# Kernel tuning notes

Hardware: AMD Instinct MI355X
Metric: run time of the kernel (lower is better)

The kernel has to match this reference:

```python
import jax, jax.numpy as jnp
import numpy as np
from functools import partial

B, C, D, H, W = 2, 96, 64, 64, 64
HALF = C // 2
EPS = 1e-5


def _dwconv3d(x, w, b):
    # x: [B, half, D, H, W]; w: [half, 1, 3, 3, 3] depthwise; b: [half]
    y = jax.lax.conv_general_dilated(
        x, w, window_strides=(1, 1, 1), padding=((1, 1), (1, 1), (1, 1)),
        dimension_numbers=('NCDHW', 'OIDHW', 'NCDHW'),
        feature_group_count=x.shape[1])
    return y + b[None, :, None, None, None]


def _conv1x1(x, w, b):
    # pointwise conv == channel GEMM; w: [Cout, Cin], b: [Cout]
    return jnp.einsum('oc,bcdhw->bodhw', w, x) + b[None, :, None, None, None]


def setup_inputs() -> dict:
    key = jax.random.key(0)
    ks = jax.random.split(key, 12)
    s = 0.02
    return {
        'x': jax.random.normal(ks[0], (B, C, D, H, W), dtype=jnp.float32),
        'norm_gamma': jnp.ones((C,), jnp.float32),
        'norm_beta': jnp.zeros((C,), jnp.float32),
        'in_w': jax.random.normal(ks[1], (C, C), jnp.float32) * s,
        'in_b': jnp.zeros((C,), jnp.float32),
        'conv_ssm_w': jax.random.normal(ks[2], (HALF, 1, 3, 3, 3), jnp.float32) * s,
        'conv_ssm_b': jnp.zeros((HALF,), jnp.float32),
        'mamba_w': jax.random.normal(ks[3], (HALF, 1, 3, 3, 3), jnp.float32) * s,
        'mamba_b': jnp.zeros((HALF,), jnp.float32),
        'conv_sym_w': jax.random.normal(ks[4], (HALF, 1, 3, 3, 3), jnp.float32) * s,
        'conv_sym_b': jnp.zeros((HALF,), jnp.float32),
        'out_w': jax.random.normal(ks[5], (C, C), jnp.float32) * s,
        'out_b': jnp.zeros((C,), jnp.float32),
    }


def reference(x, norm_gamma, norm_beta, in_w, in_b,
              conv_ssm_w, conv_ssm_b, mamba_w, mamba_b,
              conv_sym_w, conv_sym_b, out_w, out_b):
    residual = x
    # InstanceNorm3d (affine): normalize over spatial dims per (batch, channel)
    mean = jnp.mean(x, axis=(2, 3, 4), keepdims=True)
    var = jnp.var(x, axis=(2, 3, 4), keepdims=True)
    xn = (x - mean) * jax.lax.rsqrt(var + EPS)
    xn = xn * norm_gamma[None, :, None, None, None] + norm_beta[None, :, None, None, None]
    # shared 1x1 projection then split into two branches
    xp = _conv1x1(xn, in_w, in_b)
    x1, x2 = xp[:, :HALF], xp[:, HALF:]
    # SSM path: depthwise conv -> SiLU -> (fallback) depthwise conv 'mamba'
    x1 = jax.nn.silu(_dwconv3d(x1, conv_ssm_w, conv_ssm_b))
    x1 = _dwconv3d(x1, mamba_w, mamba_b)
    # symmetric conv path
    x2 = jax.nn.silu(_dwconv3d(x2, conv_sym_w, conv_sym_b))
    out = _conv1x1(jnp.concatenate([x1, x2], axis=1), out_w, out_b)
    return out + residual
```

## Files before the change

### kernel.cpp

```cpp
#include <hip/hip_runtime.h>
#include <hip/hip_bf16.h>

using u16 = unsigned short;
using u32 = unsigned int;
typedef __attribute__((ext_vector_type(8))) short bf16x8;
typedef __attribute__((ext_vector_type(4))) float f32x4;

#define DEVFN __device__ __forceinline__

static constexpr int Sn = 64*64*64;
static constexpr float EPS_ = 1e-5f;

DEVFN float lo2f(u32 u){ union { u32 i; float f; } v; v.i = u << 16; return v.f; }
DEVFN float hi2f(u32 u){ union { u32 i; float f; } v; v.i = u & 0xffff0000u; return v.f; }
DEVFN float b2f(u16 u){ union { u32 i; float f; } v; v.i = ((u32)u) << 16; return v.f; }
DEVFN u16 f2b(float f){
  union { float f; u32 i; } v; v.f = f;
  u32 r = v.i + 0x7fffu + ((v.i >> 16) & 1u);
  return (u16)(r >> 16);
}
DEVFN void unpack8(uint4 v, float* f){
  f[0]=lo2f(v.x); f[1]=hi2f(v.x);
  f[2]=lo2f(v.y); f[3]=hi2f(v.y);
  f[4]=lo2f(v.z); f[5]=hi2f(v.z);
  f[6]=lo2f(v.w); f[7]=hi2f(v.w);
}
DEVFN void unpack4(uint2 v, float* f){
  f[0]=lo2f(v.x); f[1]=hi2f(v.x);
  f[2]=lo2f(v.y); f[3]=hi2f(v.y);
}
DEVFN void load8f(const float* p, float* f){
  float4 a = *reinterpret_cast<const float4*>(p);
  float4 b = *reinterpret_cast<const float4*>(p + 4);
  f[0]=a.x; f[1]=a.y; f[2]=a.z; f[3]=a.w;
  f[4]=b.x; f[5]=b.y; f[6]=b.z; f[7]=b.w;
}

__global__ __launch_bounds__(256) void k_stats_partial(
    const float* __restrict__ x, float2* __restrict__ psum, u16* __restrict__ xb){
  int bid = blockIdx.x;
  int bc = bid >> 2, chunk = bid & 3;
  size_t base = (size_t)bc * Sn + (size_t)chunk * (Sn/4);
  const float* p = x + base;
  u16* q = xb + base;
  float s = 0.f, s2 = 0.f;
  int t = threadIdx.x;
  #pragma unroll 4
  for (int k = 0; k < 32; ++k){
    size_t off = (size_t)k*2048 + t*8;
    float f[8]; load8f(p + off, f);
    u16 ob[8];
    #pragma unroll
    for (int j=0;j<8;j++){ s += f[j]; s2 += f[j]*f[j]; ob[j] = f2b(f[j]); }
    *reinterpret_cast<uint4*>(q + off) = *reinterpret_cast<const uint4*>(ob);
  }
  #pragma unroll
  for (int off=32; off; off>>=1){ s += __shfl_down(s, off); s2 += __shfl_down(s2, off); }
  __shared__ float rs[4], rs2[4];
  int wid = t >> 6;
  if ((t & 63) == 0){ rs[wid]=s; rs2[wid]=s2; }
  __syncthreads();
  if (t == 0){
    psum[bid] = make_float2(rs[0]+rs[1]+rs[2]+rs[3], rs2[0]+rs2[1]+rs2[2]+rs2[3]);
  }
}

__global__ __launch_bounds__(192) void k_fold(
    const float2* __restrict__ psum,
    const float* __restrict__ gamma, const float* __restrict__ beta,
    const float* __restrict__ in_w, const float* __restrict__ in_b,
    const float* __restrict__ out_w,
    u16* __restrict__ W2pad ,
    u16* __restrict__ W3pad ,
    float* __restrict__ bias2 ){
  __shared__ float scl[192], shf[192];
  int t = threadIdx.x;
  {
    float s=0.f, s2=0.f;
    #pragma unroll
    for (int k=0;k<4;k++){ float2 v = psum[t*4+k]; s += v.x; s2 += v.y; }
    float inv = 1.f / (float)Sn;
    float mean = s * inv;
    float var  = s2 * inv - mean*mean;
    int c = t % 96;
    float sc = gamma[c] * rsqrtf(var + EPS_);
    scl[t] = sc;
    shf[t] = beta[c] - mean * sc;
  }
  __syncthreads();
  int b = t / 96, o = t % 96;
  float acc = in_b[o];
  for (int c=0;c<96;c++){
    float w = in_w[o*96 + c];
    int bc = b*96 + c;
    W2pad[(size_t)(b*96 + o)*104 + c] = f2b(w * scl[bc]);
    acc += w * shf[bc];
  }
  bias2[t] = acc;
  if (t < 96){
    for (int c=0;c<96;c++)
      W3pad[(size_t)t*104 + c] = f2b(out_w[t*96 + c]);
  }
}

template<int MODE>
__global__ __launch_bounds__(256, 4) void k_gemm(
    const u16*  __restrict__ xb,
    const u16*  __restrict__ y1,
    const u16*  __restrict__ y2,
    const u16*  __restrict__ Wpad,
    const float* __restrict__ bias,
    u16* __restrict__ dst16,
    float* __restrict__ dst32){
  __shared__ __attribute__((aligned(16))) u16 lds[18432];
  u16* Wl = lds;
  u16* X  = lds + 9984;
  const int t  = threadIdx.x;
  const int b  = blockIdx.x >> 12;
  const int s0 = (blockIdx.x & 4095) << 6;

  {
    const uint4* wsrc = reinterpret_cast<const uint4*>(Wpad + (MODE==0 ? (size_t)b*9984 : 0));
    uint4* wdst = reinterpret_cast<uint4*>(lds);
    #pragma unroll
    for (int i=0;i<5;i++){ int idx = i*256 + t; if (idx < 1248) wdst[idx] = wsrc[idx]; }
  }

  #pragma unroll
  for (int it=0; it<2; ++it){
    int task = it*256 + t;
    if (task < 384){
      int sp = task & 31, cblk = task >> 5;
      int s = sp*2;
      u16 rA[8], rB[8];
      #pragma unroll
      for (int j=0;j<8;j++){
        int c = cblk*8 + j;
        const u16* src;
        if (MODE==0)      src = xb + ((size_t)(b*96 + c))*Sn;
        else if (c < 48)  src = y1 + ((size_t)(b*48 + c))*Sn;
        else              src = y2 + ((size_t)(b*48 + (c-48)))*Sn;
        u32 v = *reinterpret_cast<const u32*>(src + s0 + s);
        rA[j] = (u16)v; rB[j] = (u16)(v >> 16);
      }
      *reinterpret_cast<uint4*>(&X[(size_t)s*132 + cblk*8]) = *reinterpret_cast<const uint4*>(rA);
      *reinterpret_cast<uint2*>(&X[(size_t)(s+1)*132 + cblk*8])     = *reinterpret_cast<const uint2*>(&rB[0]);
      *reinterpret_cast<uint2*>(&X[(size_t)(s+1)*132 + cblk*8 + 4]) = *reinterpret_cast<const uint2*>(&rB[4]);
    }
  }
  __syncthreads();

  const int w  = t >> 6;
  const int l  = t & 63;
  const int lc = l & 15, lr = l >> 4;

  f32x4 acc[6];
  #pragma unroll
  for (int m=0;m<6;m++)
    #pragma unroll
    for (int r=0;r<4;r++) acc[m][r] = 0.f;

  #pragma unroll
  for (int kk=0; kk<3; ++kk){
    const int kb = kk*4 + lr;
    bf16x8 xv;
    {
      const u16* px = &X[(size_t)(w*16 + lc)*132 + kb*8];
      uint2 p0 = *reinterpret_cast<const uint2*>(px);
      uint2 p1 = *reinterpret_cast<const uint2*>(px + 4);
      union { uint4 u; bf16x8 v; } cv;
      cv.u = make_uint4(p0.x, p0.y, p1.x, p1.y);
      xv = cv.v;
    }
    #pragma unroll
    for (int m=0;m<6;m++){
      bf16x8 a = *reinterpret_cast<const bf16x8*>(&Wl[(size_t)(16*m + lc)*104 + kb*8]);
      acc[m] = __builtin_amdgcn_mfma_f32_16x16x32_bf16(a, xv, acc[m], 0, 0, 0);
    }
  }
  __syncthreads();

  if (MODE==0){
    u16* eps = lds;
    #pragma unroll
    for (int m=0;m<6;m++){
      #pragma unroll
      for (int r=0;r<4;r++){
        int o = 16*m + lr*4 + r;
        eps[(size_t)o*72 + w*16 + lc] = f2b(acc[m][r] + bias[b*96 + o]);
      }
    }
    __syncthreads();
    #pragma unroll
    for (int i=0;i<3;i++){
      int idx = i*256 + t;
      int o = idx >> 3, qq = idx & 7;
      *reinterpret_cast<uint4*>(dst16 + ((size_t)(b*96 + o))*Sn + s0 + qq*8) =
          *reinterpret_cast<const uint4*>(&eps[(size_t)o*72 + qq*8]);
    }
  } else {
    float* eps = reinterpret_cast<float*>(lds);
    #pragma unroll
    for (int m=0;m<6;m++){
      #pragma unroll
      for (int r=0;r<4;r++){
        int o = 16*m + lr*4 + r;
        eps[(size_t)o*68 + w*16 + lc] = acc[m][r] + bias[o];
      }
    }
    __syncthreads();
    #pragma unroll
    for (int i=0;i<6;i++){
      int idx = i*256 + t;
      int o = idx >> 4, qq = idx & 15;
      size_t off = ((size_t)(b*96 + o))*Sn + s0 + qq*4;
      float4 v  = *reinterpret_cast<const float4*>(&eps[(size_t)o*68 + qq*4]);
      uint2 rv = *reinterpret_cast<const uint2*>(xb + off);
      float rf[4]; unpack4(rv, rf);
      v.x += rf[0]; v.y += rf[1]; v.z += rf[2]; v.w += rf[3];
      *reinterpret_cast<float4*>(dst32 + off) = v;
    }
  }
}

template<int SILU>
__global__ __launch_bounds__(256) void k_dw(
    const u16* __restrict__ src, int sCPB, int sCOff,
    u16* __restrict__ dst, int dCPB, int dCOff,
    const float* __restrict__ wts , const float* __restrict__ bias){
  int hw = blockIdx.x;
  int id = (hw & 7)*768 + (hw >> 3);
  int d = id & 63; int c = (id >> 6) % 48; int b = id / (48*64);
  int t = threadIdx.x;
  int h = t >> 2, w0 = (t & 3) * 16;
  float wf[27];
  const float* wp = wts + c*27;
  #pragma unroll
  for (int k=0;k<27;k++) wf[k] = wp[k];
  float acc[16];
  float bv = bias[c];
  #pragma unroll
  for (int j=0;j<16;j++) acc[j] = bv;
  const u16* sp = src + ((size_t)(b*sCPB + sCOff + c)) * Sn;
  #pragma unroll
  for (int dd=-1; dd<=1; dd++){
    int zd = d + dd; if (zd < 0 || zd > 63) continue;
    #pragma unroll
    for (int dh=-1; dh<=1; dh++){
      int zh = h + dh; if (zh < 0 || zh > 63) continue;
      const u16* row = sp + zd*4096 + zh*64 + w0;
      float m[16];
      unpack8(*reinterpret_cast<const uint4*>(row), m);
      unpack8(*reinterpret_cast<const uint4*>(row+8), m+8);
      float rl = __shfl_up(m[15], 1);
      float rr = __shfl_down(m[0], 1);
      if ((t & 3) == 0) rl = 0.f;
      if ((t & 3) == 3) rr = 0.f;
      const float* wk = &wf[(dd+1)*9 + (dh+1)*3];
      #pragma unroll
      for (int j=0;j<16;j++){
        float L = (j==0)  ? rl : m[j-1];
        float R = (j==15) ? rr : m[j+1];
        acc[j] += wk[0]*L + wk[1]*m[j] + wk[2]*R;
      }
    }
  }
  u16 ob[16];
  #pragma unroll
  for (int j=0;j<16;j++){
    float v = acc[j];
    if (SILU) v = v / (1.f + __expf(-v));
    ob[j] = f2b(v);
  }
  u16* dp = dst + ((size_t)(b*dCPB + dCOff + c)) * Sn + d*4096 + h*64 + w0;
  *reinterpret_cast<uint4*>(dp)   = *reinterpret_cast<const uint4*>(&ob[0]);
  *reinterpret_cast<uint4*>(dp+8) = *reinterpret_cast<const uint4*>(&ob[8]);
}

extern "C" void kernel_launch(void* const* d_in, const int* in_sizes, int n_in,
                              void* d_out, int out_size, void* d_ws, size_t ws_size,
                              hipStream_t stream){
  const float* x      = (const float*)d_in[0];
  const float* gamma  = (const float*)d_in[1];
  const float* beta   = (const float*)d_in[2];
  const float* in_w   = (const float*)d_in[3];
  const float* in_b   = (const float*)d_in[4];
  const float* ssm_w  = (const float*)d_in[5];
  const float* ssm_b  = (const float*)d_in[6];
  const float* mam_w  = (const float*)d_in[7];
  const float* mam_b  = (const float*)d_in[8];
  const float* sym_w  = (const float*)d_in[9];
  const float* sym_b  = (const float*)d_in[10];
  const float* out_w  = (const float*)d_in[11];
  const float* out_b  = (const float*)d_in[12];
  float* out = (float*)d_out;

  u16* du16 = (u16*)d_out;

  char* ws = (char*)d_ws;
  u16*    y2    = (u16*)ws;
  u16*    y1    = (u16*)(ws + 50331648);
  u16*    xb    = (u16*)(ws + 100663296);
  float2* psum  = (float2*)(ws + 201326592);
  u16*    W2pad = (u16*)(ws + 201326592 + 6144);
  u16*    W3pad = (u16*)(ws + 201326592 + 6144 + 39936);
  float*  bias2 = (float*)(ws + 201326592 + 6144 + 39936 + 19968);

  k_stats_partial<<<768, 256, 0, stream>>>(x, psum, xb);
  k_fold<<<1, 192, 0, stream>>>(psum, gamma, beta, in_w, in_b, out_w, W2pad, W3pad, bias2);
  k_gemm<0><<<8192, 256, 0, stream>>>(xb, nullptr, nullptr, W2pad, bias2, du16, nullptr);
  k_dw<1><<<6144, 256, 0, stream>>>(du16, 96, 48, y2, 48, 0, sym_w, sym_b);
  k_dw<1><<<6144, 256, 0, stream>>>(du16, 96, 0,  du16, 96, 192, ssm_w, ssm_b);
  k_dw<0><<<6144, 256, 0, stream>>>(du16, 96, 192, y1, 48, 0, mam_w, mam_b);
  k_gemm<1><<<8192, 256, 0, stream>>>(xb, y1, y2, W3pad, out_b, nullptr, out);
}
```

Baseline: 363.3 us.

## Stage depthwise conv halos in LDS, merge two dwconv launches, parallelize fold

The depthwise 3D conv kernel now loads three zero-padded depth planes into shared memory as fp32 and reads the 3x3 neighbourhood from LDS, where before each thread issued repeated global loads per tap and used shuffles for the edges. The first-stage ssm and sym depthwise convs are merged into one launch over 96 channels, with outputs routed to the right buffers. The single-block fold kernel is spread over 288 blocks, with a shared-memory reduction for the bias. The cost is a large LDS footprint per block, about 54KB, which limits occupancy, plus extra zero-fill and staging work.

```diff
diff --git a/kernel.cpp b/kernel.cpp
--- a/kernel.cpp
+++ b/kernel.cpp
@@ -65,7 +65,7 @@
   }
 }
 
-__global__ __launch_bounds__(192) void k_fold(
+__global__ __launch_bounds__(96) void k_fold(
     const float2* __restrict__ psum,
     const float* __restrict__ gamma, const float* __restrict__ beta,
     const float* __restrict__ in_w, const float* __restrict__ in_b,
@@ -73,33 +73,31 @@
     u16* __restrict__ W2pad ,
     u16* __restrict__ W3pad ,
     float* __restrict__ bias2 ){
-  __shared__ float scl[192], shf[192];
-  int t = threadIdx.x;
-  {
+  int blk = blockIdx.x;
+  int c = threadIdx.x;
+  if (blk < 192){
+    int b = blk / 96, o = blk - (blk/96)*96;
     float s=0.f, s2=0.f;
     #pragma unroll
-    for (int k=0;k<4;k++){ float2 v = psum[t*4+k]; s += v.x; s2 += v.y; }
+    for (int k=0;k<4;k++){ float2 v = psum[(b*96 + c)*4 + k]; s += v.x; s2 += v.y; }
     float inv = 1.f / (float)Sn;
     float mean = s * inv;
     float var  = s2 * inv - mean*mean;
-    int c = t % 96;
     float sc = gamma[c] * rsqrtf(var + EPS_);
-    scl[t] = sc;
-    shf[t] = beta[c] - mean * sc;
-  }
-  __syncthreads();
-  int b = t / 96, o = t % 96;
-  float acc = in_b[o];
-  for (int c=0;c<96;c++){
+    float sh = beta[c] - mean * sc;
     float w = in_w[o*96 + c];
-    int bc = b*96 + c;
-    W2pad[(size_t)(b*96 + o)*104 + c] = f2b(w * scl[bc]);
-    acc += w * shf[bc];
-  }
-  bias2[t] = acc;
-  if (t < 96){
-    for (int c=0;c<96;c++)
-      W3pad[(size_t)t*104 + c] = f2b(out_w[t*96 + c]);
+    W2pad[(size_t)(b*96 + o)*104 + c] = f2b(w * sc);
+    __shared__ float red[96];
+    red[c] = w * sh;
+    __syncthreads();
+    if (c == 0){
+      float a = in_b[o];
+      for (int i=0;i<96;i++) a += red[i];
+      bias2[b*96 + o] = a;
+    }
+  } else {
+    int o = blk - 192;
+    W3pad[(size_t)o*104 + c] = f2b(out_w[o*96 + c]);
   }
 }
 
@@ -223,15 +221,54 @@
   }
 }
 
-template<int SILU>
-__global__ __launch_bounds__(256) void k_dw(
+template<int SILU, int MERGED>
+__global__ __launch_bounds__(256) void k_dwl(
     const u16* __restrict__ src, int sCPB, int sCOff,
     u16* __restrict__ dst, int dCPB, int dCOff,
-    const float* __restrict__ wts , const float* __restrict__ bias){
+    u16* __restrict__ dst2,
+    const float* __restrict__ wtsA, const float* __restrict__ biasA,
+    const float* __restrict__ wtsB, const float* __restrict__ biasB){
   int hw = blockIdx.x;
-  int id = (hw & 7)*768 + (hw >> 3);
-  int d = id & 63; int c = (id >> 6) % 48; int b = id / (48*64);
-  int t = threadIdx.x;
+  int nchunk = MERGED ? 1536 : 768;
+  int id = (hw & 7)*nchunk + (hw >> 3);
+  int CC = MERGED ? 96 : 48;
+  int d = id & 63; int cc = (id >> 6) % CC; int b = id / (CC*64);
+  bool sym = MERGED && (cc >= 48);
+  int c = sym ? (cc - 48) : cc;
+  const float* wts  = sym ? wtsB  : wtsA;
+  const float* bias = sym ? biasB : biasA;
+  const int t = threadIdx.x;
+
+  __shared__ float S[4 + 3*66*68];
+
+  if (t < 4) S[t] = 0.f;
+  for (int z = t; z < 408; z += 256){
+    int s = z / 136, rm = z - s*136;
+    int r = (rm >= 68) ? 65 : 0; int wd = (rm >= 68) ? (rm - 68) : rm;
+    S[4 + s*4488 + r*68 + wd] = 0.f;
+  }
+  for (int z = t; z < 768; z += 256){
+    int s = z >> 8, i = z & 255; int h = i >> 2, wd = 64 + (i & 3);
+    S[4 + s*4488 + (h+1)*68 + wd] = 0.f;
+  }
+
+  const u16* plane = src + ((size_t)(b*sCPB + sCOff + cc)) * Sn;
+  #pragma unroll
+  for (int it = 0; it < 6; ++it){
+    int k = it*256 + t;
+    int s = k >> 9, i = k & 511;
+    int h = i >> 3, w8 = (i & 7) << 3;
+    int zd = d - 1 + s;
+    uint4 v = make_uint4(0u,0u,0u,0u);
+    if (zd >= 0 && zd <= 63)
+      v = *reinterpret_cast<const uint4*>(plane + zd*4096 + h*64 + w8);
+    float f[8]; unpack8(v, f);
+    float* q = &S[4 + s*4488 + (h+1)*68 + w8];
+    *reinterpret_cast<float4*>(q)   = *reinterpret_cast<const float4*>(&f[0]);
+    *reinterpret_cast<float4*>(q+4) = *reinterpret_cast<const float4*>(&f[4]);
+  }
+  __syncthreads();
+
   int h = t >> 2, w0 = (t & 3) * 16;
   float wf[27];
   const float* wp = wts + c*27;
@@ -241,22 +278,19 @@
   float bv = bias[c];
   #pragma unroll
   for (int j=0;j<16;j++) acc[j] = bv;
-  const u16* sp = src + ((size_t)(b*sCPB + sCOff + c)) * Sn;
-  #pragma unroll
-  for (int dd=-1; dd<=1; dd++){
-    int zd = d + dd; if (zd < 0 || zd > 63) continue;
-    #pragma unroll
-    for (int dh=-1; dh<=1; dh++){
-      int zh = h + dh; if (zh < 0 || zh > 63) continue;
-      const u16* row = sp + zd*4096 + zh*64 + w0;
+
+  #pragma unroll
+  for (int s=0;s<3;s++){
+    #pragma unroll
+    for (int dh=0;dh<3;dh++){
+      const float* row = &S[4 + s*4488 + (h+dh)*68 + w0];
       float m[16];
-      unpack8(*reinterpret_cast<const uint4*>(row), m);
-      unpack8(*reinterpret_cast<const uint4*>(row+8), m+8);
-      float rl = __shfl_up(m[15], 1);
-      float rr = __shfl_down(m[0], 1);
-      if ((t & 3) == 0) rl = 0.f;
-      if ((t & 3) == 3) rr = 0.f;
-      const float* wk = &wf[(dd+1)*9 + (dh+1)*3];
+      #pragma unroll
+      for (int q=0;q<4;q++)
+        *reinterpret_cast<float4*>(&m[q*4]) = *reinterpret_cast<const float4*>(row + q*4);
+      float rl = row[-1];
+      float rr = row[16];
+      const float* wk = &wf[s*9 + dh*3];
       #pragma unroll
       for (int j=0;j<16;j++){
         float L = (j==0)  ? rl : m[j-1];
@@ -265,6 +299,7 @@
       }
     }
   }
+
   u16 ob[16];
   #pragma unroll
   for (int j=0;j<16;j++){
@@ -272,7 +307,9 @@
     if (SILU) v = v / (1.f + __expf(-v));
     ob[j] = f2b(v);
   }
-  u16* dp = dst + ((size_t)(b*dCPB + dCOff + c)) * Sn + d*4096 + h*64 + w0;
+  u16* dp;
+  if (MERGED && sym) dp = dst2 + ((size_t)(b*48 + c)) * Sn + d*4096 + h*64 + w0;
+  else               dp = dst  + ((size_t)(b*dCPB + dCOff + c)) * Sn + d*4096 + h*64 + w0;
   *reinterpret_cast<uint4*>(dp)   = *reinterpret_cast<const uint4*>(&ob[0]);
   *reinterpret_cast<uint4*>(dp+8) = *reinterpret_cast<const uint4*>(&ob[8]);
 }
@@ -307,10 +344,9 @@
   float*  bias2 = (float*)(ws + 201326592 + 6144 + 39936 + 19968);
 
   k_stats_partial<<<768, 256, 0, stream>>>(x, psum, xb);
-  k_fold<<<1, 192, 0, stream>>>(psum, gamma, beta, in_w, in_b, out_w, W2pad, W3pad, bias2);
+  k_fold<<<288, 96, 0, stream>>>(psum, gamma, beta, in_w, in_b, out_w, W2pad, W3pad, bias2);
   k_gemm<0><<<8192, 256, 0, stream>>>(xb, nullptr, nullptr, W2pad, bias2, du16, nullptr);
-  k_dw<1><<<6144, 256, 0, stream>>>(du16, 96, 48, y2, 48, 0, sym_w, sym_b);
-  k_dw<1><<<6144, 256, 0, stream>>>(du16, 96, 0,  du16, 96, 192, ssm_w, ssm_b);
-  k_dw<0><<<6144, 256, 0, stream>>>(du16, 96, 192, y1, 48, 0, mam_w, mam_b);
+  k_dwl<1,1><<<12288, 256, 0, stream>>>(du16, 96, 0, du16, 96, 192, y2, ssm_w, ssm_b, sym_w, sym_b);
+  k_dwl<0,0><<<6144, 256, 0, stream>>>(du16, 96, 192, y1, 48, 0, nullptr, mam_w, mam_b, nullptr, nullptr);
   k_gemm<1><<<8192, 256, 0, stream>>>(xb, y1, y2, W3pad, out_b, nullptr, out);
 }
```

Result: slower. 498.3 us (+37.2%).
